# Kernel tuning notes

Hardware: AMD Instinct MI355X
Metric: run time of the kernel (lower is better)

Reference implementation:

```python
import jax, jax.numpy as jnp
import numpy as np

B, S, D, H, L, DFF = 32, 512, 1024, 16, 4, 2048
DK = D // H
NEG = -1e32
EPS = 1e-5


def setup_inputs() -> dict:
    key = jax.random.key(0)
    ks = jax.random.split(key, 8)
    std = 0.02
    inp = {
        "q_embed": jax.random.normal(ks[0], (B, S, D), jnp.float32),
        "qa_embed": jax.random.normal(ks[1], (B, S, D), jnp.float32),
        # per-block stacked params [L, ...]; torch Linear stored as [in, out]
        "Wk": jax.random.normal(ks[2], (L, D, D), jnp.float32) * std,
        "bk": jnp.zeros((L, D), jnp.float32),
        "Wv": jax.random.normal(ks[3], (L, D, D), jnp.float32) * std,
        "bv": jnp.zeros((L, D), jnp.float32),
        "Wo": jax.random.normal(ks[4], (L, D, D), jnp.float32) * std,
        "bo": jnp.zeros((L, D), jnp.float32),
        "ln1_s": jnp.ones((L, D), jnp.float32),
        "ln1_b": jnp.zeros((L, D), jnp.float32),
        "W1": jax.random.normal(ks[5], (L, D, DFF), jnp.float32) * std,
        "b1": jnp.zeros((L, DFF), jnp.float32),
        "W2": jax.random.normal(ks[6], (L, DFF, D), jnp.float32) * std,
        "b2": jnp.zeros((L, D), jnp.float32),
        "ln2_s": jnp.ones((L, D), jnp.float32),
        "ln2_b": jnp.zeros((L, D), jnp.float32),
    }
    return inp


def _ln(x, s, b):
    m = jnp.mean(x, axis=-1, keepdims=True)
    v = jnp.mean((x - m) ** 2, axis=-1, keepdims=True)
    return (x - m) / jnp.sqrt(v + EPS) * s + b


def _block(x, y, Wk, bk, Wv, bv, Wo, bo, l1s, l1b, W1, b1, W2, b2, l2s, l2b, allowed):
    # kq_same=1: q and k both use k_linear; q == k since query == key == x
    qk = (x @ Wk + bk).reshape(B, S, H, DK).transpose(0, 2, 1, 3)  # [B,H,S,DK]
    v = (y @ Wv + bv).reshape(B, S, H, DK).transpose(0, 2, 1, 3)
    scores = jnp.einsum("bhid,bhjd->bhij", qk, qk) / np.sqrt(DK)
    scores = jnp.where(allowed, scores, NEG)  # strictly-causal mask
    attn = jax.nn.softmax(scores, axis=-1)
    attn = attn * (jnp.arange(S)[None, None, :, None] > 0)  # zero_pad row 0
    o = jnp.einsum("bhij,bhjd->bhid", attn, v)  # [B,H,S,DK]
    o = o.transpose(0, 2, 1, 3).reshape(B, S, D) @ Wo + bo
    x = _ln(x + o, l1s, l1b)
    f = jax.nn.relu(x @ W1 + b1) @ W2 + b2
    return _ln(x + f, l2s, l2b)


def reference(q_embed, qa_embed, Wk, bk, Wv, bv, Wo, bo, ln1_s, ln1_b,
              W1, b1, W2, b2, ln2_s, ln2_b):
    allowed = jnp.tril(jnp.ones((S, S), bool), -1)  # j < i
    x, y = q_embed, qa_embed
    for i in range(L):
        x = _block(x, y, Wk[i], bk[i], Wv[i], bv[i], Wo[i], bo[i],
                   ln1_s[i], ln1_b[i], W1[i], b1[i], W2[i], b2[i],
                   ln2_s[i], ln2_b[i], allowed)
    return x
```

## Files before the change

### kernel.cpp

```cpp
#include <hip/hip_runtime.h>

#define B_ 32
#define S_ 512
#define D_ 1024
#define H_ 16
#define DK_ 64
#define DFF_ 2048
#define L_ 4

typedef __attribute__((ext_vector_type(8))) short short8;
typedef __attribute__((ext_vector_type(4))) float f32x4;
typedef unsigned short u16;
typedef unsigned int u32;
typedef __attribute__((ext_vector_type(4))) u16 u16x4;
typedef __attribute__((ext_vector_type(8))) u16 u16x8;

__device__ __forceinline__ u16 f2bf(float f) {
    u32 u = __float_as_uint(f);
    u = u + 0x7fffu + ((u >> 16) & 1u);
    return (u16)(u >> 16);
}
__device__ __forceinline__ u16 f2bf_t(float f) {
    return (u16)(__float_as_uint(f) >> 16);
}
__device__ __forceinline__ float bf2f(u16 v) {
    return __uint_as_float(((u32)v) << 16);
}

__device__ __forceinline__ void async16(const u16* g, u16* l) {
    __builtin_amdgcn_global_load_lds((const __attribute__((address_space(1))) u32*)g,
                                     (__attribute__((address_space(3))) u32*)l, 16, 0, 0);
}

#define RD_A2(dst, CBX, MP, CHV)                                               \
    dst[0] = *(const short8*)&lds[(CBX) + arow + (2*(MP)+0)*1024 + (CHV)];     \
    dst[1] = *(const short8*)&lds[(CBX) + arow + (2*(MP)+1)*1024 + (CHV)];

#define RD_B4(dst, CBX, CHV)                                                   \
    _Pragma("unroll")                                                          \
    for (int ni = 0; ni < 4; ni++)                                             \
        dst[ni] = *(const short8*)&lds[32768 + (CBX) + browr + ni*1024 + (CHV)];

#define MF8(MP, ASRC, BSRC, LGN)                                               \
    asm volatile("s_waitcnt lgkmcnt(" #LGN ")" ::: "memory");                  \
    __builtin_amdgcn_sched_barrier(0);                                         \
    __builtin_amdgcn_s_setprio(1);                                             \
    _Pragma("unroll")                                                          \
    for (int ni = 0; ni < 4; ni++) {                                           \
        acc[2*(MP)+0][ni] = __builtin_amdgcn_mfma_f32_16x16x32_bf16(           \
            ASRC[0], BSRC[ni], acc[2*(MP)+0][ni], 0, 0, 0);                    \
        acc[2*(MP)+1][ni] = __builtin_amdgcn_mfma_f32_16x16x32_bf16(           \
            ASRC[1], BSRC[ni], acc[2*(MP)+1][ni], 0, 0, 0);                    \
    }                                                                          \
    __builtin_amdgcn_s_setprio(0);                                             \
    __builtin_amdgcn_s_barrier();                                              \
    __builtin_amdgcn_sched_barrier(0);

template<int RELU, int OUTM>
__global__ __launch_bounds__(512, 2)
void gemm256(const u16* __restrict__ A, const u16* __restrict__ Bt,
             const float* __restrict__ bias, void* __restrict__ C,
             int M, int N, int K)
{
    __shared__ __align__(16) u16 lds[65536];
    const int t = threadIdx.x;
    const int w = t >> 6, l = t & 63;
    const int lane16 = l & 15, quad = l >> 4;
    const int wm = w >> 2, wn = w & 3;

    const int gx = gridDim.x;
    const int nwg = gx * gridDim.y;
    const int orig = blockIdx.y * gx + blockIdx.x;
    const int q8 = nwg >> 3, r8 = nwg & 7;
    const int xcd = orig & 7, sidx = orig >> 3;
    const int nid = (xcd < r8 ? xcd * (q8 + 1) : r8 * (q8 + 1) + (xcd - r8) * q8) + sidx;
    const int m0 = (nid / gx) * 256;
    const int n0 = (nid % gx) * 256;

    f32x4 acc[8][4];
#pragma unroll
    for (int i = 0; i < 8; i++)
#pragma unroll
        for (int j = 0; j < 4; j++) acc[i][j] = f32x4{0.f, 0.f, 0.f, 0.f};

    const int lr = l >> 3;
    const int xorcol = ((l & 7) ^ lr) * 8;
    const int aw8 = (w < 4 ? w * 8 : 128 + (w - 4) * 8);
    const u16* Asrc = A + (size_t)(m0 + aw8 + lr) * K + xorcol;
    const u16* Bsrc = Bt + (size_t)(n0 + w * 8 + lr) * K + xorcol;

    auto stageA = [&](int tile, int q) {
        const int c = tile & 1;
        async16(Asrc + (size_t)(q * 32) * K + (tile << 6),
                &lds[c * 16384 + (aw8 + q * 32) * 64]);
    };
    auto stageB = [&](int tile, int j) {
        const int c = tile & 1;
        async16(Bsrc + (size_t)(j * 64) * K + (tile << 6),
                &lds[32768 + c * 16384 + (j * 64 + w * 8) * 64]);
    };

    const int chv0 = ((0 + quad) ^ (lane16 & 7)) * 8;
    const int chv1 = ((4 + quad) ^ (lane16 & 7)) * 8;
    const int arow  = (wm * 128 + lane16) * 64;
    const int browr = (wn * 64 + lane16) * 64;

    const int NT = K >> 6;

    stageA(0, 0); stageB(0, 0); stageA(0, 1); stageB(0, 1);
    stageA(0, 2); stageB(0, 2); stageA(0, 3); stageB(0, 3);
    stageA(1, 0); stageB(1, 0); stageA(1, 1); stageB(1, 1);
    stageA(1, 2); stageB(1, 2);
    asm volatile("s_waitcnt vmcnt(6)" ::: "memory");
    __builtin_amdgcn_sched_barrier(0);
    __builtin_amdgcn_s_barrier();

    short8 a0[2], a1[2], bk0[4], bk1[4];
    RD_B4(bk0, 0, chv0)
    RD_A2(a0, 0, 0, chv0)

    for (int tt = 0; tt < NT; tt++) {
        const int cb  = (tt & 1) << 14;
        const int cbn = ((tt + 1) & 1) << 14;
        const bool hn1 = (tt + 1 < NT);
        const bool hn2 = (tt + 2 < NT);

        RD_A2(a1, cb, 1, chv0)
        MF8(0, a0, bk0, 2)
        if (hn1) { stageA(tt + 1, 3); stageB(tt + 1, 3); }
        RD_A2(a0, cb, 2, chv0)
        bk1[0] = *(const short8*)&lds[32768 + cb + browr + 0 * 1024 + chv1];
        bk1[1] = *(const short8*)&lds[32768 + cb + browr + 1 * 1024 + chv1];
        MF8(1, a1, bk0, 4)
        RD_A2(a1, cb, 3, chv0)
        bk1[2] = *(const short8*)&lds[32768 + cb + browr + 2 * 1024 + chv1];
        bk1[3] = *(const short8*)&lds[32768 + cb + browr + 3 * 1024 + chv1];
        MF8(2, a0, bk0, 6)
        RD_A2(a0, cb, 0, chv1)
        MF8(3, a1, bk0, 4)
        RD_A2(a1, cb, 1, chv1)
        MF8(0, a0, bk1, 2)
        if (hn2) { stageA(tt + 2, 0); stageB(tt + 2, 0); }
        RD_A2(a0, cb, 2, chv1)
        MF8(1, a1, bk1, 2)
        if (hn2) { stageA(tt + 2, 1); stageB(tt + 2, 1); }
        RD_A2(a1, cb, 3, chv1)
        MF8(2, a0, bk1, 2)
        if (hn2) { stageA(tt + 2, 2); stageB(tt + 2, 2); }
        if (hn2) asm volatile("s_waitcnt vmcnt(6)" ::: "memory");
        else     asm volatile("s_waitcnt vmcnt(0)" ::: "memory");
        __builtin_amdgcn_sched_barrier(0);
        __builtin_amdgcn_s_barrier();
        __builtin_amdgcn_sched_barrier(0);
        if (hn1) {
            RD_B4(bk0, cbn, chv0)
            RD_A2(a0, cbn, 0, chv0)
            MF8(3, a1, bk1, 6)
        } else {
            MF8(3, a1, bk1, 0)
        }
    }

#pragma unroll
    for (int mi = 0; mi < 8; mi++) {
#pragma unroll
        for (int ni = 0; ni < 4; ni++) {
            int col = n0 + wn * 64 + ni * 16 + lane16;
            float bv = bias[col];
            if (OUTM == 2) {
                int tok0 = m0 + wm * 128 + mi * 16 + quad * 4;
                int bb = tok0 >> 9, s0 = tok0 & 511;
                int hh = col >> 6, dd = col & 63;
                u16x4 pk;
#pragma unroll
                for (int r2 = 0; r2 < 4; r2++) pk[r2] = f2bf(acc[mi][ni][r2] + bv);
                *(u16x4*)&((u16*)C)[(((size_t)bb * H_ + hh) * DK_ + dd) * S_ + s0] = pk;
            } else {
                int row = m0 + wm * 128 + mi * 16 + quad * 4;
#pragma unroll
                for (int r2 = 0; r2 < 4; r2++) {
                    float v = acc[mi][ni][r2] + bv;
                    if (RELU) v = fmaxf(v, 0.f);
                    size_t idx = (size_t)(row + r2) * N + col;
                    if (OUTM == 1) ((u16*)C)[idx] = f2bf(v);
                    else           ((float*)C)[idx] = v;
                }
            }
        }
    }
}

__global__ __launch_bounds__(256, 3)
void attn_kernel(const u16* __restrict__ qk, const u16* __restrict__ vt,
                 u16* __restrict__ ao)
{
    __shared__ __align__(16) u16 sP[4][32 * 72];
    const int t = threadIdx.x, w = t >> 6, l = t & 63;
    const int lane16 = l & 15, quad = l >> 4;
    const int p = blockIdx.x;
    const int bh = blockIdx.y;
    const int b = bh >> 4, h = bh & 15;
    const int band = (w < 2) ? (2 * p + w) : (15 - 2 * p - (w - 2));
    const int band0 = band * 32;
    const u16* kb = qk + (size_t)b * S_ * D_ + h * DK_;
    const u16* vb = vt + (size_t)bh * DK_ * S_;
    u16* aob = ao + (size_t)b * S_ * D_ + h * DK_;
    const float SC = 0.125f * 1.44269504f;
    u16* myP = sP[w];

    short8 bq[2][2];
#pragma unroll
    for (int ii = 0; ii < 2; ii++)
#pragma unroll
        for (int kf = 0; kf < 2; kf++)
            bq[ii][kf] = *(const short8*)(kb + (size_t)(band0 + ii * 16 + lane16) * D_ +
                                          kf * 32 + quad * 8);

    f32x4 aco[4][2];
    float lsum[2] = {0.f, 0.f};
#pragma unroll
    for (int di = 0; di < 4; di++)
#pragma unroll
        for (int ii = 0; ii < 2; ii++) aco[di][ii] = f32x4{0.f, 0.f, 0.f, 0.f};

    const int ntiles = (band >> 1) + 1;
    for (int jt = 0; jt < ntiles; jt++) {
        const int j0 = jt * 64;
        const bool diag = (jt == ntiles - 1);

        short8 aK[2][4];
#pragma unroll
        for (int kf = 0; kf < 2; kf++)
#pragma unroll
            for (int ji = 0; ji < 4; ji++)
                aK[kf][ji] = *(const short8*)(kb + (size_t)(j0 + ji * 16 + lane16) * D_ +
                                              kf * 32 + quad * 8);
        f32x4 sacc[4][2];
#pragma unroll
        for (int ji = 0; ji < 4; ji++)
#pragma unroll
            for (int ii = 0; ii < 2; ii++) sacc[ji][ii] = f32x4{0.f, 0.f, 0.f, 0.f};
#pragma unroll
        for (int kf = 0; kf < 2; kf++)
#pragma unroll
            for (int ji = 0; ji < 4; ji++)
#pragma unroll
                for (int ii = 0; ii < 2; ii++)
                    sacc[ji][ii] = __builtin_amdgcn_mfma_f32_16x16x32_bf16(
                        aK[kf][ji], bq[ii][kf], sacc[ji][ii], 0, 0, 0);

        short8 aV[2][4];
#pragma unroll
        for (int kf = 0; kf < 2; kf++)
#pragma unroll
            for (int di = 0; di < 4; di++)
                aV[kf][di] = *(const short8*)(vb + (size_t)(di * 16 + lane16) * S_ +
                                              j0 + kf * 32 + quad * 8);

#pragma unroll
        for (int ii = 0; ii < 2; ii++) {
#pragma unroll
            for (int ji = 0; ji < 4; ji++) {
                u16x4 pk;
#pragma unroll
                for (int r2 = 0; r2 < 4; r2++) {
                    float v = sacc[ji][ii][r2] * SC;
                    if (diag) {
                        int j = j0 + ji * 16 + quad * 4 + r2;
                        int i = band0 + ii * 16 + lane16;
                        if (j >= i) v = -3e38f;
                    }
                    float pv = exp2f(v);
                    lsum[ii] += pv;
                    pk[r2] = f2bf_t(pv);
                }
                *(u16x4*)&myP[(ii * 16 + lane16) * 72 + ji * 16 + quad * 4] = pk;
            }
        }

        short8 pf[2][2];
#pragma unroll
        for (int kf = 0; kf < 2; kf++)
#pragma unroll
            for (int ii = 0; ii < 2; ii++)
                pf[kf][ii] = *(const short8*)&myP[(ii * 16 + lane16) * 72 +
                                                  kf * 32 + quad * 8];
#pragma unroll
        for (int kf = 0; kf < 2; kf++)
#pragma unroll
            for (int di = 0; di < 4; di++)
#pragma unroll
                for (int ii = 0; ii < 2; ii++)
                    aco[di][ii] = __builtin_amdgcn_mfma_f32_16x16x32_bf16(
                        aV[kf][di], pf[kf][ii], aco[di][ii], 0, 0, 0);
    }

#pragma unroll
    for (int ii = 0; ii < 2; ii++) {
        lsum[ii] += __shfl_xor(lsum[ii], 16);
        lsum[ii] += __shfl_xor(lsum[ii], 32);
    }

#pragma unroll
    for (int ii = 0; ii < 2; ii++) {
        int row = band0 + ii * 16 + lane16;
        float lv = lsum[ii];
        float inv = (row == 0 || !(lv > 0.f)) ? 0.f : 1.f / lv;
#pragma unroll
        for (int di = 0; di < 4; di++) {
            u16x4 o;
#pragma unroll
            for (int r2 = 0; r2 < 4; r2++) o[r2] = f2bf(aco[di][ii][r2] * inv);
            *(u16x4*)&aob[(size_t)row * D_ + di * 16 + quad * 4] = o;
        }
    }
}

template<int XBF, int WF32>
__global__ __launch_bounds__(256)
void ln_kernel(const void* __restrict__ xin, const float* __restrict__ addv,
               const float* __restrict__ sc, const float* __restrict__ bi,
               u16* __restrict__ xb_out, float* __restrict__ f32_out)
{
    const int row = blockIdx.x;
    const int t = threadIdx.x;
    const int w = t >> 6, l = t & 63;
    __shared__ float red[8];
    f32x4 a;
    if (XBF) {
        u16x4 raw = ((const u16x4*)xin)[(size_t)row * 256 + t];
#pragma unroll
        for (int j = 0; j < 4; j++) a[j] = bf2f(raw[j]);
    } else {
        a = ((const f32x4*)xin)[(size_t)row * 256 + t];
    }
    f32x4 c = ((const f32x4*)(addv + (size_t)row * D_))[t];
    f32x4 v;
    float s1 = 0.f, s2 = 0.f;
#pragma unroll
    for (int j = 0; j < 4; j++) {
        v[j] = a[j] + c[j];
        s1 += v[j];
        s2 += v[j] * v[j];
    }
#pragma unroll
    for (int off = 32; off > 0; off >>= 1) {
        s1 += __shfl_xor(s1, off);
        s2 += __shfl_xor(s2, off);
    }
    if (l == 0) { red[w * 2] = s1; red[w * 2 + 1] = s2; }
    __syncthreads();
    s1 = red[0] + red[2] + red[4] + red[6];
    s2 = red[1] + red[3] + red[5] + red[7];
    float mean = s1 * (1.f / D_);
    float var = s2 * (1.f / D_) - mean * mean;
    float rstd = rsqrtf(var + 1e-5f);
    f32x4 s4 = ((const f32x4*)sc)[t];
    f32x4 b4 = ((const f32x4*)bi)[t];
    f32x4 o;
    u16x4 ob;
#pragma unroll
    for (int j = 0; j < 4; j++) {
        o[j] = (v[j] - mean) * rstd * s4[j] + b4[j];
        ob[j] = f2bf(o[j]);
    }
    ((u16x4*)(xb_out + (size_t)row * D_))[t] = ob;
    if (WF32) ((f32x4*)(f32_out + (size_t)row * D_))[t] = o;
}

__global__ void cvt_kernel(const float* __restrict__ in, u16* __restrict__ out, int n4)
{
    int i = blockIdx.x * blockDim.x + threadIdx.x;
    if (i < n4) {
        f32x4 v = ((const f32x4*)in)[i];
        u16x4 o;
#pragma unroll
        for (int j = 0; j < 4; j++) o[j] = f2bf(v[j]);
        ((u16x4*)out)[i] = o;
    }
}

__device__ __forceinline__ void tconv_body(const float* W, u16* WT, int K, int N,
                                           int bx, int by, int t)
{
    __shared__ float tile[64][65];
    const int n0 = bx * 64, k0 = by * 64;
#pragma unroll
    for (int i = 0; i < 4; i++) {
        int kr = (t >> 4) + i * 16;
        int nc = (t & 15) * 4;
        f32x4 v = *(const f32x4*)&W[(size_t)(k0 + kr) * N + n0 + nc];
        tile[kr][nc] = v[0]; tile[kr][nc + 1] = v[1];
        tile[kr][nc + 2] = v[2]; tile[kr][nc + 3] = v[3];
    }
    __syncthreads();
#pragma unroll
    for (int i = 0; i < 4; i++) {
        int nr = (t >> 4) + i * 16;
        int kc = (t & 15) * 4;
        u16x4 o;
#pragma unroll
        for (int j = 0; j < 4; j++) o[j] = f2bf(tile[kc + j][nr]);
        *(u16x4*)&WT[(size_t)(n0 + nr) * K + k0 + kc] = o;
    }
}

__global__ __launch_bounds__(256)
void wconv_kernel(const float* __restrict__ Wk, const float* __restrict__ Wv,
                  const float* __restrict__ Wo, const float* __restrict__ W1f,
                  const float* __restrict__ W2f,
                  u16* __restrict__ wk, u16* __restrict__ wv, u16* __restrict__ wo,
                  u16* __restrict__ w1, u16* __restrict__ w2)
{
    const int idx = blockIdx.x;
    const float* W; u16* T; int K, N, bx, by;
    if (idx < 768) {
        int wsel = idx >> 8, t16 = idx & 255;
        W = (wsel == 0) ? Wk : (wsel == 1) ? Wv : Wo;
        T = (wsel == 0) ? wk : (wsel == 1) ? wv : wo;
        K = 1024; N = 1024; bx = t16 & 15; by = t16 >> 4;
    } else if (idx < 1280) {
        int i = idx - 768;
        W = W1f; T = w1; K = 1024; N = 2048; bx = i & 31; by = i >> 5;
    } else {
        int i = idx - 1280;
        W = W2f; T = w2; K = 2048; N = 1024; bx = i & 15; by = i >> 4;
    }
    tconv_body(W, T, K, N, bx, by, threadIdx.x);
}

extern "C" void kernel_launch(void* const* d_in, const int* in_sizes, int n_in,
                              void* d_out, int out_size, void* d_ws, size_t ws_size,
                              hipStream_t stream)
{
    const float* q_embed = (const float*)d_in[0];
    const float* qa_embed = (const float*)d_in[1];
    const float* Wk = (const float*)d_in[2];
    const float* bk = (const float*)d_in[3];
    const float* Wv = (const float*)d_in[4];
    const float* bv = (const float*)d_in[5];
    const float* Wo = (const float*)d_in[6];
    const float* bo = (const float*)d_in[7];
    const float* ln1_s = (const float*)d_in[8];
    const float* ln1_b = (const float*)d_in[9];
    const float* W1 = (const float*)d_in[10];
    const float* b1 = (const float*)d_in[11];
    const float* W2 = (const float*)d_in[12];
    const float* b2 = (const float*)d_in[13];
    const float* ln2_s = (const float*)d_in[14];
    const float* ln2_b = (const float*)d_in[15];
    (void)in_sizes; (void)n_in; (void)out_size;

    char* ws = (char*)d_ws;
    size_t off = 0;
    auto carve = [&](size_t bytes) -> char* {
        char* p = ws + off;
        off += (bytes + 255) & ~(size_t)255;
        return p;
    };
    const size_t NTOK = (size_t)B_ * S_;
    u16* wk = (u16*)carve((size_t)D_ * D_ * 2);
    u16* wv = (u16*)carve((size_t)D_ * D_ * 2);
    u16* wo = (u16*)carve((size_t)D_ * D_ * 2);
    u16* w1 = (u16*)carve((size_t)D_ * DFF_ * 2);
    u16* w2 = (u16*)carve((size_t)DFF_ * D_ * 2);
    u16* x = (u16*)carve(NTOK * D_ * 2);
    u16* U12 = (u16*)carve(NTOK * DFF_ * 2);
    u16* U3 = (u16*)carve(NTOK * D_ * 2);
    size_t off_overlay = off;
    u16* ybf_sep = (u16*)carve(NTOK * D_ * 2);
    bool sep = (ws_size >= off);
    if (!sep) off = off_overlay;
    if (ws_size < off) return;

    u16* qkb = U12;
    u16* vbf = U12 + NTOK * D_;
    u16* hb = U12;
    u16* aob = U3;
    u16* ybf = sep ? ybf_sep : U3;
    float* of32 = (float*)d_out;

    cvt_kernel<<<16384, 256, 0, stream>>>(q_embed, x, (int)(NTOK * D_ / 4));
    if (sep)
        cvt_kernel<<<16384, 256, 0, stream>>>(qa_embed, ybf, (int)(NTOK * D_ / 4));

    const dim3 G1024(4, 64), G2048(8, 64);
    for (int lyr = 0; lyr < L_; lyr++) {
        const size_t wsq = (size_t)lyr * D_ * D_;
        const size_t wf1 = (size_t)lyr * D_ * DFF_;
        wconv_kernel<<<1792, 256, 0, stream>>>(Wk + wsq, Wv + wsq, Wo + wsq,
                                               W1 + wf1, W2 + wf1,
                                               wk, wv, wo, w1, w2);
        if (!sep)
            cvt_kernel<<<16384, 256, 0, stream>>>(qa_embed, ybf, (int)(NTOK * D_ / 4));
        gemm256<0, 1><<<G1024, 512, 0, stream>>>(x, wk, bk + lyr * D_,
                                                 qkb, (int)NTOK, D_, D_);
        gemm256<0, 2><<<G1024, 512, 0, stream>>>(ybf, wv, bv + lyr * D_,
                                                 vbf, (int)NTOK, D_, D_);
        attn_kernel<<<dim3(4, B_ * H_), 256, 0, stream>>>(qkb, vbf, aob);
        gemm256<0, 0><<<G1024, 512, 0, stream>>>(aob, wo, bo + lyr * D_,
                                                 of32, (int)NTOK, D_, D_);
        if (lyr == 0)
            ln_kernel<0, 0><<<(int)NTOK, 256, 0, stream>>>(q_embed, of32,
                ln1_s + lyr * D_, ln1_b + lyr * D_, x, nullptr);
        else
            ln_kernel<1, 0><<<(int)NTOK, 256, 0, stream>>>(x, of32,
                ln1_s + lyr * D_, ln1_b + lyr * D_, x, nullptr);
        gemm256<1, 1><<<G2048, 512, 0, stream>>>(x, w1, b1 + lyr * DFF_,
                                                 hb, (int)NTOK, DFF_, D_);
        gemm256<0, 0><<<G1024, 512, 0, stream>>>(hb, w2, b2 + lyr * D_,
                                                 of32, (int)NTOK, D_, DFF_);
        if (lyr == L_ - 1)
            ln_kernel<1, 1><<<(int)NTOK, 256, 0, stream>>>(x, of32,
                ln2_s + lyr * D_, ln2_b + lyr * D_, x, (float*)d_out);
        else
            ln_kernel<1, 0><<<(int)NTOK, 256, 0, stream>>>(x, of32,
                ln2_s + lyr * D_, ln2_b + lyr * D_, x, nullptr);
    }
}
```

Before: 1.793 ms.

## Restructure GEMM main loop into 4x4 MFMA groups and prefetch K tiles in attention

The GEMM main loop moves from eight 8-MFMA groups to four 16-MFMA groups. A-fragments are read four at a time into ping-pong registers, and there are fewer barriers per K tile. The global-to-LDS staging order changes so that B tiles load first and A rows are interleaved differently. The attention kernel double-buffers its K fragments, loading the next tile's K alongside V before the score MFMAs, to hide global load latency. Together these add register pressure and change the wait/barrier placement, which could reduce occupancy or introduce LDS hazards.

After: 3.367 ms. +87.8%, slower.

```diff
diff --git a/kernel.cpp b/kernel.cpp
--- a/kernel.cpp
+++ b/kernel.cpp
@@ -32,29 +32,29 @@
                                      (__attribute__((address_space(3))) u32*)l, 16, 0, 0);
 }
 
-#define RD_A2(dst, CBX, MP, CHV)                                               \
-    dst[0] = *(const short8*)&lds[(CBX) + arow + (2*(MP)+0)*1024 + (CHV)];     \
-    dst[1] = *(const short8*)&lds[(CBX) + arow + (2*(MP)+1)*1024 + (CHV)];
+#define RD_A4(dst, CBX, MQ, CHV)                                               \
+    _Pragma("unroll")                                                          \
+    for (int mi2 = 0; mi2 < 4; mi2++)                                          \
+        dst[mi2] = *(const short8*)&lds[(CBX) + arow + ((MQ)*4 + mi2)*1024 + (CHV)];
 
 #define RD_B4(dst, CBX, CHV)                                                   \
     _Pragma("unroll")                                                          \
     for (int ni = 0; ni < 4; ni++)                                             \
         dst[ni] = *(const short8*)&lds[32768 + (CBX) + browr + ni*1024 + (CHV)];
 
-#define MF8(MP, ASRC, BSRC, LGN)                                               \
+#define MF16(ACCB, ASRC, BSRC, LGN)                                            \
     asm volatile("s_waitcnt lgkmcnt(" #LGN ")" ::: "memory");                  \
     __builtin_amdgcn_sched_barrier(0);                                         \
     __builtin_amdgcn_s_setprio(1);                                             \
     _Pragma("unroll")                                                          \
-    for (int ni = 0; ni < 4; ni++) {                                           \
-        acc[2*(MP)+0][ni] = __builtin_amdgcn_mfma_f32_16x16x32_bf16(           \
-            ASRC[0], BSRC[ni], acc[2*(MP)+0][ni], 0, 0, 0);                    \
-        acc[2*(MP)+1][ni] = __builtin_amdgcn_mfma_f32_16x16x32_bf16(           \
-            ASRC[1], BSRC[ni], acc[2*(MP)+1][ni], 0, 0, 0);                    \
+    for (int mi2 = 0; mi2 < 4; mi2++) {                                        \
+        _Pragma("unroll")                                                      \
+        for (int ni = 0; ni < 4; ni++) {                                       \
+            acc[(ACCB)+mi2][ni] = __builtin_amdgcn_mfma_f32_16x16x32_bf16(     \
+                ASRC[mi2], BSRC[ni], acc[(ACCB)+mi2][ni], 0, 0, 0);            \
+        }                                                                      \
     }                                                                          \
-    __builtin_amdgcn_s_setprio(0);                                             \
-    __builtin_amdgcn_s_barrier();                                              \
-    __builtin_amdgcn_sched_barrier(0);
+    __builtin_amdgcn_s_setprio(0);
 
 template<int RELU, int OUTM>
 __global__ __launch_bounds__(512, 2)
@@ -107,17 +107,18 @@
 
     const int NT = K >> 6;
 
-    stageA(0, 0); stageB(0, 0); stageA(0, 1); stageB(0, 1);
-    stageA(0, 2); stageB(0, 2); stageA(0, 3); stageB(0, 3);
-    stageA(1, 0); stageB(1, 0); stageA(1, 1); stageB(1, 1);
-    stageA(1, 2); stageB(1, 2);
+    stageA(0, 0); stageA(0, 1); stageA(0, 2); stageA(0, 3);
+    stageB(0, 0); stageB(0, 1); stageB(0, 2); stageB(0, 3);
+    stageB(1, 0); stageB(1, 1); stageB(1, 2); stageB(1, 3);
+    stageA(1, 0); stageA(1, 2);
     asm volatile("s_waitcnt vmcnt(6)" ::: "memory");
     __builtin_amdgcn_sched_barrier(0);
     __builtin_amdgcn_s_barrier();
-
-    short8 a0[2], a1[2], bk0[4], bk1[4];
-    RD_B4(bk0, 0, chv0)
-    RD_A2(a0, 0, 0, chv0)
+    __builtin_amdgcn_sched_barrier(0);
+
+    short8 aping[4], apong[4], b0[4], b1[4];
+    RD_B4(b0, 0, chv0)
+    RD_A4(aping, 0, 0, chv0)
 
     for (int tt = 0; tt < NT; tt++) {
         const int cb  = (tt & 1) << 14;
@@ -125,39 +126,32 @@
         const bool hn1 = (tt + 1 < NT);
         const bool hn2 = (tt + 2 < NT);
 
-        RD_A2(a1, cb, 1, chv0)
-        MF8(0, a0, bk0, 2)
-        if (hn1) { stageA(tt + 1, 3); stageB(tt + 1, 3); }
-        RD_A2(a0, cb, 2, chv0)
-        bk1[0] = *(const short8*)&lds[32768 + cb + browr + 0 * 1024 + chv1];
-        bk1[1] = *(const short8*)&lds[32768 + cb + browr + 1 * 1024 + chv1];
-        MF8(1, a1, bk0, 4)
-        RD_A2(a1, cb, 3, chv0)
-        bk1[2] = *(const short8*)&lds[32768 + cb + browr + 2 * 1024 + chv1];
-        bk1[3] = *(const short8*)&lds[32768 + cb + browr + 3 * 1024 + chv1];
-        MF8(2, a0, bk0, 6)
-        RD_A2(a0, cb, 0, chv1)
-        MF8(3, a1, bk0, 4)
-        RD_A2(a1, cb, 1, chv1)
-        MF8(0, a0, bk1, 2)
-        if (hn2) { stageA(tt + 2, 0); stageB(tt + 2, 0); }
-        RD_A2(a0, cb, 2, chv1)
-        MF8(1, a1, bk1, 2)
-        if (hn2) { stageA(tt + 2, 1); stageB(tt + 2, 1); }
-        RD_A2(a1, cb, 3, chv1)
-        MF8(2, a0, bk1, 2)
-        if (hn2) { stageA(tt + 2, 2); stageB(tt + 2, 2); }
+        if (hn1) { stageA(tt + 1, 1); stageA(tt + 1, 3); }
+        RD_A4(apong, cb, 1, chv0)
+        RD_B4(b1, cb, chv1)
+        MF16(0, aping, b0, 8)
+        __builtin_amdgcn_s_barrier();
+        RD_A4(aping, cb, 0, chv1)
+        MF16(4, apong, b0, 8)
+        __builtin_amdgcn_s_barrier();
+        RD_A4(apong, cb, 1, chv1)
+        MF16(0, aping, b1, 4)
+        __builtin_amdgcn_s_barrier();
+        if (hn2) {
+            stageB(tt + 2, 0); stageB(tt + 2, 1); stageB(tt + 2, 2); stageB(tt + 2, 3);
+            stageA(tt + 2, 0); stageA(tt + 2, 2);
+        }
         if (hn2) asm volatile("s_waitcnt vmcnt(6)" ::: "memory");
         else     asm volatile("s_waitcnt vmcnt(0)" ::: "memory");
         __builtin_amdgcn_sched_barrier(0);
         __builtin_amdgcn_s_barrier();
         __builtin_amdgcn_sched_barrier(0);
         if (hn1) {
-            RD_B4(bk0, cbn, chv0)
-            RD_A2(a0, cbn, 0, chv0)
-            MF8(3, a1, bk1, 6)
+            RD_B4(b0, cbn, chv0)
+            RD_A4(aping, cbn, 0, chv0)
+            MF16(4, apong, b1, 8)
         } else {
-            MF8(3, a1, bk1, 0)
+            MF16(4, apong, b1, 0)
         }
     }
 
@@ -224,30 +218,18 @@
         for (int ii = 0; ii < 2; ii++) aco[di][ii] = f32x4{0.f, 0.f, 0.f, 0.f};
 
     const int ntiles = (band >> 1) + 1;
-    for (int jt = 0; jt < ntiles; jt++) {
+
+    short8 aKa[2][4], aKb[2][4];
+#pragma unroll
+    for (int kf = 0; kf < 2; kf++)
+#pragma unroll
+        for (int ji = 0; ji < 4; ji++)
+            aKa[kf][ji] = *(const short8*)(kb + (size_t)(ji * 16 + lane16) * D_ +
+                                           kf * 32 + quad * 8);
+
+    auto body = [&](int jt, short8 (&kc)[2][4], short8 (&kn)[2][4]) {
         const int j0 = jt * 64;
         const bool diag = (jt == ntiles - 1);
-
-        short8 aK[2][4];
-#pragma unroll
-        for (int kf = 0; kf < 2; kf++)
-#pragma unroll
-            for (int ji = 0; ji < 4; ji++)
-                aK[kf][ji] = *(const short8*)(kb + (size_t)(j0 + ji * 16 + lane16) * D_ +
-                                              kf * 32 + quad * 8);
-        f32x4 sacc[4][2];
-#pragma unroll
-        for (int ji = 0; ji < 4; ji++)
-#pragma unroll
-            for (int ii = 0; ii < 2; ii++) sacc[ji][ii] = f32x4{0.f, 0.f, 0.f, 0.f};
-#pragma unroll
-        for (int kf = 0; kf < 2; kf++)
-#pragma unroll
-            for (int ji = 0; ji < 4; ji++)
-#pragma unroll
-                for (int ii = 0; ii < 2; ii++)
-                    sacc[ji][ii] = __builtin_amdgcn_mfma_f32_16x16x32_bf16(
-                        aK[kf][ji], bq[ii][kf], sacc[ji][ii], 0, 0, 0);
 
         short8 aV[2][4];
 #pragma unroll
@@ -256,6 +238,28 @@
             for (int di = 0; di < 4; di++)
                 aV[kf][di] = *(const short8*)(vb + (size_t)(di * 16 + lane16) * S_ +
                                               j0 + kf * 32 + quad * 8);
+        if (!diag) {
+#pragma unroll
+            for (int kf = 0; kf < 2; kf++)
+#pragma unroll
+                for (int ji = 0; ji < 4; ji++)
+                    kn[kf][ji] = *(const short8*)(kb +
+                        (size_t)(j0 + 64 + ji * 16 + lane16) * D_ + kf * 32 + quad * 8);
+        }
+
+        f32x4 sacc[4][2];
+#pragma unroll
+        for (int ji = 0; ji < 4; ji++)
+#pragma unroll
+            for (int ii = 0; ii < 2; ii++) sacc[ji][ii] = f32x4{0.f, 0.f, 0.f, 0.f};
+#pragma unroll
+        for (int kf = 0; kf < 2; kf++)
+#pragma unroll
+            for (int ji = 0; ji < 4; ji++)
+#pragma unroll
+                for (int ii = 0; ii < 2; ii++)
+                    sacc[ji][ii] = __builtin_amdgcn_mfma_f32_16x16x32_bf16(
+                        kc[kf][ji], bq[ii][kf], sacc[ji][ii], 0, 0, 0);
 
 #pragma unroll
         for (int ii = 0; ii < 2; ii++) {
@@ -293,7 +297,14 @@
                 for (int ii = 0; ii < 2; ii++)
                     aco[di][ii] = __builtin_amdgcn_mfma_f32_16x16x32_bf16(
                         aV[kf][di], pf[kf][ii], aco[di][ii], 0, 0, 0);
-    }
+    };
+
+    int jt = 0;
+    for (; jt + 2 <= ntiles; jt += 2) {
+        body(jt, aKa, aKb);
+        body(jt + 1, aKb, aKa);
+    }
+    if (jt < ntiles) body(jt, aKa, aKb);
 
 #pragma unroll
     for (int ii = 0; ii < 2; ii++) {
```
